# Optimization experiments

Hardware: AMD Instinct MI355X
Metric: run time of the kernel (lower is better)

Reference implementation:

```python
import jax, jax.numpy as jnp
import numpy as np

B, LEN, D, N = 512, 128, 96, 128   # batch, time steps, obs dim, latent dim
NBLOCKS = 5                        # iResNet blocks in encoder/decoder


def expm_fixed(M, squarings=6, order=12):
    """Differentiable matrix exponential: scaling-and-squaring + Taylor-Horner.
    Equivalent to torch.matrix_exp for the well-conditioned skew-symmetric
    A*dt kernels used here (||A*dt|| << 2^squarings)."""
    M = M / (2.0 ** squarings)
    I = jnp.eye(M.shape[-1], dtype=M.dtype)
    P = I
    for k in range(order, 0, -1):  # Horner: I + M(I + M/2(I + ...))
        P = I + (M @ P) / k
    for _ in range(squarings):
        P = P @ P
    return P


def setup_inputs() -> dict:
    key = jax.random.key(0)
    ks = jax.random.split(key, 16)
    # strictly increasing timestamps shared across the batch
    T = jnp.cumsum(0.01 + 0.15 * jax.random.uniform(ks[0], (LEN,), dtype=jnp.float32))
    X = jax.random.normal(ks[1], (B, LEN, D), dtype=jnp.float32)
    mask = jax.random.bernoulli(ks[2], 0.5, (B, LEN, D))  # True = observed
    # skew-symmetric system kernel (kernel_initialization='skew-symmetric')
    W = jax.random.normal(ks[3], (N, N), dtype=jnp.float32) / np.sqrt(N)
    A = 0.5 * (W - W.T)
    # linear embedding d->n and projection n->d
    W_emb = jax.random.normal(ks[4], (N, D), dtype=jnp.float32) / np.sqrt(D)
    b_emb = jnp.zeros((N,), jnp.float32)
    W_proj = jax.random.normal(ks[5], (D, N), dtype=jnp.float32) / np.sqrt(N)
    b_proj = jnp.zeros((D,), jnp.float32)
    # iResNet encoder/decoder: 5 residual blocks of Linear->ReLU->Linear,
    # weights scaled small to mimic the spectral-norm contraction constraint
    cs = 0.5 / np.sqrt(N)
    enc_W1 = jax.random.normal(ks[6], (NBLOCKS, N, N), dtype=jnp.float32) * cs
    enc_b1 = jnp.zeros((NBLOCKS, N), jnp.float32)
    enc_W2 = jax.random.normal(ks[7], (NBLOCKS, N, N), dtype=jnp.float32) * cs
    enc_b2 = jnp.zeros((NBLOCKS, N), jnp.float32)
    dec_W1 = jax.random.normal(ks[8], (NBLOCKS, N, N), dtype=jnp.float32) * cs
    dec_b1 = jnp.zeros((NBLOCKS, N), jnp.float32)
    dec_W2 = jax.random.normal(ks[9], (NBLOCKS, N, N), dtype=jnp.float32) * cs
    dec_b2 = jnp.zeros((NBLOCKS, N), jnp.float32)
    # GRUCell filter: input = concat([xtilde, mask]) (2D features), hidden = D
    s = 1.0 / np.sqrt(D)
    W_ih = jax.random.uniform(ks[10], (3 * D, 2 * D), jnp.float32, -s, s)
    W_hh = jax.random.uniform(ks[11], (3 * D, D), jnp.float32, -s, s)
    b_ih = jax.random.uniform(ks[12], (3 * D,), jnp.float32, -s, s)
    b_hh = jax.random.uniform(ks[13], (3 * D,), jnp.float32, -s, s)
    return {"T": T, "X": X, "mask": mask, "A": A,
            "W_emb": W_emb, "b_emb": b_emb, "W_proj": W_proj, "b_proj": b_proj,
            "enc_W1": enc_W1, "enc_b1": enc_b1, "enc_W2": enc_W2, "enc_b2": enc_b2,
            "dec_W1": dec_W1, "dec_b1": dec_b1, "dec_W2": dec_W2, "dec_b2": dec_b2,
            "W_ih": W_ih, "W_hh": W_hh, "b_ih": b_ih, "b_hh": b_hh}


def reference(T, X, mask, A, W_emb, b_emb, W_proj, b_proj,
              enc_W1, enc_b1, enc_W2, enc_b2,
              dec_W1, dec_b1, dec_W2, dec_b2,
              W_ih, W_hh, b_ih, b_hh):
    def resnet(z, Ws1, bs1, Ws2, bs2):
        for i in range(NBLOCKS):  # fixed small depth
            z = z + jax.nn.relu(z @ Ws1[i].T + bs1[i]) @ Ws2[i].T + bs2[i]
        return z

    def gru(x, h):  # torch.nn.GRUCell math
        gi = x @ W_ih.T + b_ih
        gh = h @ W_hh.T + b_hh
        ir, iz, inn = jnp.split(gi, 3, axis=-1)
        hr, hz, hn = jnp.split(gh, 3, axis=-1)
        r = jax.nn.sigmoid(ir + hr)
        zg = jax.nn.sigmoid(iz + hz)
        ng = jnp.tanh(inn + r * hn)
        return (1.0 - zg) * ng + zg * h

    embed = lambda x: x @ W_emb.T + b_emb
    project = lambda z: z @ W_proj.T + b_proj

    dt = jnp.concatenate([jnp.zeros((1,), T.dtype), jnp.diff(T)])  # (LEN,)
    Xs = jnp.moveaxis(X, 1, 0)      # (LEN, B, D)
    Ms = jnp.moveaxis(mask, 1, 0)   # (LEN, B, D)

    # initial latent state from zero estimate
    z0 = resnet(embed(jnp.zeros((B, D), X.dtype)), enc_W1, enc_b1, enc_W2, enc_b2)

    def step(z, inp):
        dti, xi, mi = inp
        expAdt = expm_fixed(A * dti)                         # (N, N)
        zhat_pre = z @ expAdt.T                              # ODE propagate
        xhat_pre = project(resnet(zhat_pre, dec_W1, dec_b1, dec_W2, dec_b2))
        xtilde = jnp.where(mi, xi, xhat_pre)                 # impute unobserved
        u = jnp.concatenate([xtilde, mi.astype(xi.dtype)], axis=-1)  # concat_mask
        xhat_post = gru(u, xhat_pre)                         # filter update
        z_next = resnet(embed(xhat_post), enc_W1, enc_b1, enc_W2, enc_b2)
        return z_next, xhat_post

    _, Xhat = jax.lax.scan(step, z0, (dt, Xs, Ms))
    return jnp.moveaxis(Xhat, 0, 1)  # (B, LEN, D)
```

## Files before the change

### kernel.cpp

```cpp
#include <hip/hip_runtime.h>
#include <hip/hip_bf16.h>


#define NBATCH 512
#define TLEN 128
#define DDIM 96
#define NDIM 128
#define NBLK 5
#define TAYLOR 8

typedef unsigned short u16;
typedef unsigned int u32;

__device__ __forceinline__ float bf2f(u16 u){ union{u32 i; float f;} v; v.i=((u32)u)<<16; return v.f; }
__device__ __forceinline__ float lo2f(u32 w){ union{u32 i; float f;} v; v.i=w<<16; return v.f; }
__device__ __forceinline__ float hi2f(u32 w){ union{u32 i; float f;} v; v.i=w&0xFFFF0000u; return v.f; }

template<int FM>
__device__ __forceinline__ float ldf(const void* p, int i){
  if constexpr (FM==1) return ((const float*)p)[i];
  else return bf2f(((const u16*)p)[i]);
}

struct __align__(16) SMState {
  float e[NDIM];
  float V0[NDIM];
  float V1[NDIM];
  float zh[NDIM];
  float h[NDIM];
  float xpre[DDIM];
  float u[2*DDIM];
  float gi[3*DDIM];
  float gh[3*DDIM];
  float xpost[DDIM];
};

#define A_STRIDE_E 136

template<int FM, int S, int NO, bool WL, class EPI>
__device__ __forceinline__ void mv(const void* __restrict__ Wg, const u16* __restrict__ Wl,
                                   const int ldw, const float* __restrict__ in,
                                   const int kq, const int j0, EPI epi)
{
  constexpr int NC = S/8;
  float a[S];
  {
    const float* p = in + 8*kq;
#pragma unroll
    for (int ci=0; ci<NC; ci++){
      float4 v0 = *(const float4*)(p + 32*ci);
      float4 v1 = *(const float4*)(p + 32*ci + 4);
      a[8*ci+0]=v0.x; a[8*ci+1]=v0.y; a[8*ci+2]=v0.z; a[8*ci+3]=v0.w;
      a[8*ci+4]=v1.x; a[8*ci+5]=v1.y; a[8*ci+6]=v1.z; a[8*ci+7]=v1.w;
    }
  }
  constexpr int P = (NO+63)/64;
  constexpr bool full = (NO%64==0);
#pragma unroll
  for (int pp=0; pp<P; pp++){
    const int j = pp*64 + j0;
    const bool act = full || (j < NO);
    float ac0=0.f, ac1=0.f, ac2=0.f, ac3=0.f;
    if (act){
      if constexpr (WL){
        const char* wr = (const char*)Wl + 2*(size_t)j*A_STRIDE_E + 16*kq;
#pragma unroll
        for (int ci=0; ci<NC; ci++){
          const uint4 w = *(const uint4*)(wr + 64*ci);
          float f;
          f=lo2f(w.x); ac0=fmaf(f,a[8*ci+0],ac0);
          f=hi2f(w.x); ac1=fmaf(f,a[8*ci+1],ac1);
          f=lo2f(w.y); ac2=fmaf(f,a[8*ci+2],ac2);
          f=hi2f(w.y); ac3=fmaf(f,a[8*ci+3],ac3);
          f=lo2f(w.z); ac0=fmaf(f,a[8*ci+4],ac0);
          f=hi2f(w.z); ac1=fmaf(f,a[8*ci+5],ac1);
          f=lo2f(w.w); ac2=fmaf(f,a[8*ci+6],ac2);
          f=hi2f(w.w); ac3=fmaf(f,a[8*ci+7],ac3);
        }
      } else if constexpr (FM==1){
        const float* wr = (const float*)Wg + (size_t)j*ldw + 8*kq;
#pragma unroll
        for (int ci=0; ci<NC; ci++){
          const float4 w0 = *(const float4*)(wr + 32*ci);
          const float4 w1 = *(const float4*)(wr + 32*ci + 4);
          ac0=fmaf(w0.x,a[8*ci+0],ac0); ac1=fmaf(w0.y,a[8*ci+1],ac1);
          ac2=fmaf(w0.z,a[8*ci+2],ac2); ac3=fmaf(w0.w,a[8*ci+3],ac3);
          ac0=fmaf(w1.x,a[8*ci+4],ac0); ac1=fmaf(w1.y,a[8*ci+5],ac1);
          ac2=fmaf(w1.z,a[8*ci+6],ac2); ac3=fmaf(w1.w,a[8*ci+7],ac3);
        }
      } else {
        const u16* wr = (const u16*)Wg + (size_t)j*ldw + 8*kq;
#pragma unroll
        for (int ci=0; ci<NC; ci++){
          const uint4 w = *(const uint4*)(wr + 32*ci);
          float f;
          f=lo2f(w.x); ac0=fmaf(f,a[8*ci+0],ac0);
          f=hi2f(w.x); ac1=fmaf(f,a[8*ci+1],ac1);
          f=lo2f(w.y); ac2=fmaf(f,a[8*ci+2],ac2);
          f=hi2f(w.y); ac3=fmaf(f,a[8*ci+3],ac3);
          f=lo2f(w.z); ac0=fmaf(f,a[8*ci+4],ac0);
          f=hi2f(w.z); ac1=fmaf(f,a[8*ci+5],ac1);
          f=lo2f(w.w); ac2=fmaf(f,a[8*ci+6],ac2);
          f=hi2f(w.w); ac3=fmaf(f,a[8*ci+7],ac3);
        }
      }
    }
    float acc = (ac0+ac1)+(ac2+ac3);
    acc += __shfl_xor(acc,1,64); acc += __shfl_xor(acc,2,64);
    if (act && kq==0) epi(j, acc);
  }
  __syncthreads();
}

template<int FM>
__device__ __forceinline__ void run_all(
    SMState& sm, u16* Ash, const int mode,
    const void* Tp, const void* Xp, const void* Mp, const void* Ap,
    const void* Wemb, const void* bemb, const void* Wproj, const void* bproj,
    const void* eW1, const void* eb1, const void* eW2, const void* eb2,
    const void* dW1, const void* db1, const void* dW2, const void* db2,
    const void* Wih, const void* Whh, const void* bih, const void* bhh,
    void* Out)
{
  const int tid  = threadIdx.x;
  const int lane = tid & 63;
  const int kq   = lane & 3;
  const int j0   = (tid>>6)*16 + (lane>>2);
  const int r0   = blockIdx.x;
  constexpr int WB = NDIM*NDIM*(FM?4:2);

  if constexpr (FM==0){
    const uint4* src = (const uint4*)Ap;
    for (int i=tid; i<2048; i+=256){
      const int row = i>>4, c = i&15;
      *(uint4*)((char*)Ash + 2*(size_t)row*A_STRIDE_E + 16*c) = src[i];
    }
  }

  if (tid < NDIM) sm.e[tid] = ldf<FM>(bemb, tid);
  __syncthreads();
#pragma unroll 1
  for (int ib=0; ib<NBLK; ib++){
    const void* W1 = (const char*)eW1 + (size_t)ib*WB;
    const void* W2 = (const char*)eW2 + (size_t)ib*WB;
    const int bo = ib*NDIM;
    mv<FM,32,128,false>(W1, nullptr, NDIM, sm.e, kq, j0, [&](int j,float s){
      sm.h[j]=fmaxf(s+ldf<FM>(eb1,bo+j),0.f); });
    mv<FM,32,128,false>(W2, nullptr, NDIM, sm.h, kq, j0, [&](int j,float s){
      sm.e[j]+=s+ldf<FM>(eb2,bo+j); });
  }

#pragma unroll 1
  for (int t=0; t<TLEN; t++){
    float dtv = 0.f;
    if (t > 0) dtv = ldf<FM>(Tp,t) - ldf<FM>(Tp,t-1);

    if (tid < NDIM){ const float z = sm.e[tid]; sm.V0[tid]=z; sm.zh[tid]=z; }
    __syncthreads();

#pragma unroll 1
    for (int k=1; k<=TAYLOR; k++){
      const float sc = dtv / (float)k;
      const float* Vin = (k&1) ? sm.V0 : sm.V1;
      float*      Vout = (k&1) ? sm.V1 : sm.V0;
      if constexpr (FM==0){
        mv<FM,32,128,true>(nullptr, Ash, NDIM, Vin, kq, j0, [&](int j,float s){
          const float v=s*sc; Vout[j]=v; sm.zh[j]+=v; });
      } else {
        mv<FM,32,128,false>(Ap, nullptr, NDIM, Vin, kq, j0, [&](int j,float s){
          const float v=s*sc; Vout[j]=v; sm.zh[j]+=v; });
      }
    }

#pragma unroll 1
    for (int ib=0; ib<NBLK; ib++){
      const void* W1 = (const char*)dW1 + (size_t)ib*WB;
      const void* W2 = (const char*)dW2 + (size_t)ib*WB;
      const int bo = ib*NDIM;
      mv<FM,32,128,false>(W1, nullptr, NDIM, sm.zh, kq, j0, [&](int j,float s){
        sm.h[j]=fmaxf(s+ldf<FM>(db1,bo+j),0.f); });
      mv<FM,32,128,false>(W2, nullptr, NDIM, sm.h, kq, j0, [&](int j,float s){
        sm.zh[j]+=s+ldf<FM>(db2,bo+j); });
    }

    mv<FM,32,96,false>(Wproj, nullptr, NDIM, sm.zh, kq, j0, [&](int j,float s){
      sm.xpre[j]=s+ldf<FM>(bproj,j); });

    if (tid < DDIM){
      const int d = tid;
      const size_t idx = (size_t)r0*TLEN*DDIM + (size_t)t*DDIM + d;
      bool m;
      if      (mode==0) m = ((const u16*)Mp)[idx] != 0;
      else if (mode==1) m = ((const u32*)Mp)[idx] != 0;
      else if (mode==2) m = ((const unsigned char*)Mp)[idx] != 0;
      else              m = ((const int*)Mp)[idx] != 0;
      const float xv = ldf<FM>(Xp, (int)idx);
      sm.u[d]        = m ? xv : sm.xpre[d];
      sm.u[DDIM + d] = m ? 1.f : 0.f;
    }
    __syncthreads();

    mv<FM,48,288,false>(Wih, nullptr, 2*DDIM, sm.u, kq, j0, [&](int j,float s){
      sm.gi[j]=s+ldf<FM>(bih,j); });
    mv<FM,24,288,false>(Whh, nullptr, DDIM, sm.xpre, kq, j0, [&](int j,float s){
      sm.gh[j]=s+ldf<FM>(bhh,j); });

    if (tid < DDIM){
      const int d = tid;
      const float ir=sm.gi[d], iz=sm.gi[DDIM+d], in_=sm.gi[2*DDIM+d];
      const float hr=sm.gh[d], hz=sm.gh[DDIM+d], hn=sm.gh[2*DDIM+d];
      const float rg = 1.f/(1.f+__expf(-(ir+hr)));
      const float zg = 1.f/(1.f+__expf(-(iz+hz)));
      const float ag = in_ + rg*hn;
      const float e2 = __expf(2.f*ag);
      const float ng = 1.f - 2.f/(e2+1.f);
      const float xp = sm.xpre[d];
      const float xq = (1.f-zg)*ng + zg*xp;
      sm.xpost[d] = xq;
      const size_t idx = (size_t)r0*TLEN*DDIM + (size_t)t*DDIM + d;
      if constexpr (FM==1) ((float*)Out)[idx] = xq;
      else ((__hip_bfloat16*)Out)[idx] = __float2bfloat16(xq);
    }
    __syncthreads();

    mv<FM,24,128,false>(Wemb, nullptr, DDIM, sm.xpost, kq, j0, [&](int j,float s){
      sm.e[j]=s+ldf<FM>(bemb,j); });

#pragma unroll 1
    for (int ib=0; ib<NBLK; ib++){
      const void* W1 = (const char*)eW1 + (size_t)ib*WB;
      const void* W2 = (const char*)eW2 + (size_t)ib*WB;
      const int bo = ib*NDIM;
      mv<FM,32,128,false>(W1, nullptr, NDIM, sm.e, kq, j0, [&](int j,float s){
        sm.h[j]=fmaxf(s+ldf<FM>(eb1,bo+j),0.f); });
      mv<FM,32,128,false>(W2, nullptr, NDIM, sm.h, kq, j0, [&](int j,float s){
        sm.e[j]+=s+ldf<FM>(eb2,bo+j); });
    }
  }
}

__global__ __launch_bounds__(256, 2)
void linode_kernel(const void* Tp, const void* Xp, const void* Mp, const void* Ap,
                   const void* Wemb, const void* bemb, const void* Wproj, const void* bproj,
                   const void* eW1, const void* eb1, const void* eW2, const void* eb2,
                   const void* dW1, const void* db1, const void* dW2, const void* db2,
                   const void* Wih, const void* Whh, const void* bih, const void* bhh,
                   void* Out)
{
  __shared__ SMState sm;
  __shared__ __align__(16) u16 Ash[NDIM*A_STRIDE_E];
  __shared__ int s_f[4];
  const int tid = threadIdx.x;

  if (tid < 4) s_f[tid] = 0;
  __syncthreads();
  if (tid == 0){
    int all0 = 1;
    for (int k=0; k<8; k++) all0 &= (((const u32*)Ap)[129*k] == 0u);
    s_f[3] = all0;
  }
  {
    const u32* mw = (const u32*)Mp;
    int fb=0, ff=0, fg=0;
    for (int i=tid; i<2048; i+=256){
      const u32 w = mw[i];
      if (w == 0x3F803F80u) fb = 1;
      if ((w&0xFFFFu)==0x3F80u || (w>>16)==0x3F80u) ff = 1;
      if (w > 1u) fg = 1;
    }
    if (fb) atomicOr(&s_f[0],1);
    if (ff) atomicOr(&s_f[1],1);
    if (fg) atomicOr(&s_f[2],1);
  }
  __syncthreads();
  const int mode = s_f[0] ? 0 : (s_f[1] ? 1 : (s_f[2] ? 2 : 3));
  const int f32m = s_f[3];
  __syncthreads();

  if (f32m)
    run_all<1>(sm, Ash, mode, Tp, Xp, Mp, Ap, Wemb, bemb, Wproj, bproj,
               eW1, eb1, eW2, eb2, dW1, db1, dW2, db2, Wih, Whh, bih, bhh, Out);
  else
    run_all<0>(sm, Ash, mode, Tp, Xp, Mp, Ap, Wemb, bemb, Wproj, bproj,
               eW1, eb1, eW2, eb2, dW1, db1, dW2, db2, Wih, Whh, bih, bhh, Out);
}

extern "C" void kernel_launch(void* const* d_in, const int* in_sizes, int n_in,
                              void* d_out, int out_size, void* d_ws, size_t ws_size,
                              hipStream_t stream)
{
  (void)in_sizes; (void)n_in; (void)out_size; (void)d_ws; (void)ws_size;
  hipLaunchKernelGGL(linode_kernel, dim3(NBATCH), dim3(256), 0, stream,
                     d_in[0], d_in[1], d_in[2], d_in[3],
                     d_in[4], d_in[5], d_in[6], d_in[7],
                     d_in[8], d_in[9], d_in[10], d_in[11],
                     d_in[12], d_in[13], d_in[14], d_in[15],
                     d_in[16], d_in[17], d_in[18], d_in[19],
                     d_out);
}
```

Baseline: 5.743 ms.

## Precompute per-step matrix exponentials in a separate kernel and widen blocks to 512 threads

Adds a kernel that builds each time step's truncated-Taylor expm(A*dt) in bf16 into workspace. The main recurrence then replaces eight Taylor matvecs per step with a single matvec against the precomputed matrix. The main kernel moves from 256 to 512 threads per block, which halves the output rows per thread in mv. All biases are staged into shared memory, and mask and X loads are issued early in each step. The cost is an extra launch plus a 4 MB workspace read per step, and the propagator is rounded to bf16, which changes numerics slightly.

```diff
diff --git a/kernel.cpp b/kernel.cpp
--- a/kernel.cpp
+++ b/kernel.cpp
@@ -8,6 +8,7 @@
 #define NDIM 128
 #define NBLK 5
 #define TAYLOR 8
+#define A_STRIDE_E 136
 
 typedef unsigned short u16;
 typedef unsigned int u32;
@@ -15,12 +16,23 @@
 __device__ __forceinline__ float bf2f(u16 u){ union{u32 i; float f;} v; v.i=((u32)u)<<16; return v.f; }
 __device__ __forceinline__ float lo2f(u32 w){ union{u32 i; float f;} v; v.i=w<<16; return v.f; }
 __device__ __forceinline__ float hi2f(u32 w){ union{u32 i; float f;} v; v.i=w&0xFFFF0000u; return v.f; }
+__device__ __forceinline__ u16 f2bf(float x){ union{float f;u32 i;} v; v.f=x; u32 r=v.i+0x7FFF+((v.i>>16)&1); return (u16)(r>>16); }
 
 template<int FM>
 __device__ __forceinline__ float ldf(const void* p, int i){
   if constexpr (FM==1) return ((const float*)p)[i];
   else return bf2f(((const u16*)p)[i]);
 }
+
+#define OEB1 0
+#define OEB2 640
+#define ODB1 1280
+#define ODB2 1920
+#define OBEMB 2560
+#define OBPROJ 2688
+#define OBIH 2784
+#define OBHH 3072
+#define NBIAS 3360
 
 struct __align__(16) SMState {
   float e[NDIM];
@@ -35,7 +47,93 @@
   float xpost[DDIM];
 };
 
-#define A_STRIDE_E 136
+__global__ __launch_bounds__(256, 1)
+void expm_kernel(const void* Tp, const void* Ap, u16* Ews)
+{
+  __shared__ int sf;
+  __shared__ __align__(16) u16 Ash2[NDIM*A_STRIDE_E];
+  __shared__ __align__(16) float V[2][64*132];
+  const int tid = threadIdx.x;
+  if (tid==0){
+    int all0=1;
+    for (int k=0;k<8;k++) all0 &= (((const u32*)Ap)[129*k]==0u);
+    sf = all0;
+  }
+  __syncthreads();
+  if (sf) return;
+
+  const int t = blockIdx.x >> 1, half = blockIdx.x & 1;
+  float dtv = 0.f;
+  if (t>0) dtv = bf2f(((const u16*)Tp)[t]) - bf2f(((const u16*)Tp)[t-1]);
+  {
+    const uint4* src = (const uint4*)Ap;
+    for (int i=tid;i<2048;i+=256){
+      const int row=i>>4, c=i&15;
+      *(uint4*)((char*)Ash2 + 2*(size_t)row*A_STRIDE_E + 16*c) = src[i];
+    }
+  }
+  const int c2 = tid & 31, rh = tid >> 5;
+  const int j0r = rh*16;
+  const int lc0 = 2*c2, lc1 = lc0+1;
+  const int gc0 = half*64 + lc0, gc1 = gc0+1;
+
+  float acc0[16], acc1[16];
+#pragma unroll
+  for (int jj=0;jj<16;jj++){
+    const int kk = j0r+jj;
+    const float i0 = (kk==gc0)?1.f:0.f, i1 = (kk==gc1)?1.f:0.f;
+    acc0[jj]=i0; acc1[jj]=i1;
+    V[0][lc0*132+kk]=i0; V[0][lc1*132+kk]=i1;
+  }
+  __syncthreads();
+  int cur=0;
+#pragma unroll 1
+  for (int k=1;k<=8;k++){
+    const float sc = dtv/(float)k;
+    float o0[16], o1[16];
+#pragma unroll
+    for (int jj=0;jj<16;jj++){ o0[jj]=0.f; o1[jj]=0.f; }
+#pragma unroll 1
+    for (int kb=0;kb<16;kb++){
+      const float4 va0 = *(const float4*)&V[cur][lc0*132+kb*8];
+      const float4 vb0 = *(const float4*)&V[cur][lc0*132+kb*8+4];
+      const float4 va1 = *(const float4*)&V[cur][lc1*132+kb*8];
+      const float4 vb1 = *(const float4*)&V[cur][lc1*132+kb*8+4];
+      const float v0[8]={va0.x,va0.y,va0.z,va0.w,vb0.x,vb0.y,vb0.z,vb0.w};
+      const float v1[8]={va1.x,va1.y,va1.z,va1.w,vb1.x,vb1.y,vb1.z,vb1.w};
+#pragma unroll
+      for (int jj=0;jj<16;jj++){
+        const int j = j0r+jj;
+        const uint4 w = *(const uint4*)((const char*)Ash2 + 2*(size_t)j*A_STRIDE_E + 16*kb);
+        float f;
+        f=lo2f(w.x); o0[jj]=fmaf(f,v0[0],o0[jj]); o1[jj]=fmaf(f,v1[0],o1[jj]);
+        f=hi2f(w.x); o0[jj]=fmaf(f,v0[1],o0[jj]); o1[jj]=fmaf(f,v1[1],o1[jj]);
+        f=lo2f(w.y); o0[jj]=fmaf(f,v0[2],o0[jj]); o1[jj]=fmaf(f,v1[2],o1[jj]);
+        f=hi2f(w.y); o0[jj]=fmaf(f,v0[3],o0[jj]); o1[jj]=fmaf(f,v1[3],o1[jj]);
+        f=lo2f(w.z); o0[jj]=fmaf(f,v0[4],o0[jj]); o1[jj]=fmaf(f,v1[4],o1[jj]);
+        f=hi2f(w.z); o0[jj]=fmaf(f,v0[5],o0[jj]); o1[jj]=fmaf(f,v1[5],o1[jj]);
+        f=lo2f(w.w); o0[jj]=fmaf(f,v0[6],o0[jj]); o1[jj]=fmaf(f,v1[6],o1[jj]);
+        f=hi2f(w.w); o0[jj]=fmaf(f,v0[7],o0[jj]); o1[jj]=fmaf(f,v1[7],o1[jj]);
+      }
+    }
+    __syncthreads();
+#pragma unroll
+    for (int jj=0;jj<16;jj++){
+      const int j=j0r+jj;
+      const float s0=o0[jj]*sc, s1=o1[jj]*sc;
+      acc0[jj]+=s0; acc1[jj]+=s1;
+      V[cur^1][lc0*132+j]=s0; V[cur^1][lc1*132+j]=s1;
+    }
+    __syncthreads();
+    cur^=1;
+  }
+#pragma unroll
+  for (int jj=0;jj<16;jj++){
+    const int j=j0r+jj;
+    const u32 pk = (u32)f2bf(acc0[jj]) | ((u32)f2bf(acc1[jj])<<16);
+    *((u32*)(Ews + (size_t)t*NDIM*NDIM + (size_t)j*NDIM + gc0)) = pk;
+  }
+}
 
 template<int FM, int S, int NO, bool WL, class EPI>
 __device__ __forceinline__ void mv(const void* __restrict__ Wg, const u16* __restrict__ Wl,
@@ -43,6 +141,8 @@
                                    const int kq, const int j0, EPI epi)
 {
   constexpr int NC = S/8;
+  constexpr int P = (NO+127)/128;
+  constexpr bool full = (NO%128==0);
   float a[S];
   {
     const float* p = in + 8*kq;
@@ -54,11 +154,9 @@
       a[8*ci+4]=v1.x; a[8*ci+5]=v1.y; a[8*ci+6]=v1.z; a[8*ci+7]=v1.w;
     }
   }
-  constexpr int P = (NO+63)/64;
-  constexpr bool full = (NO%64==0);
 #pragma unroll
   for (int pp=0; pp<P; pp++){
-    const int j = pp*64 + j0;
+    const int j = pp*128 + j0;
     const bool act = full || (j < NO);
     float ac0=0.f, ac1=0.f, ac2=0.f, ac3=0.f;
     if (act){
@@ -113,14 +211,19 @@
 }
 
 template<int FM>
+__device__ __forceinline__ void stage_b(const void* src, float* dst, int n, int tid){
+  for (int i=tid;i<n;i+=512) dst[i] = ldf<FM>(src,i);
+}
+
+template<int FM>
 __device__ __forceinline__ void run_all(
-    SMState& sm, u16* Ash, const int mode,
+    SMState& sm, float* smb, u16* Ash, const int mode, const int useE,
     const void* Tp, const void* Xp, const void* Mp, const void* Ap,
     const void* Wemb, const void* bemb, const void* Wproj, const void* bproj,
     const void* eW1, const void* eb1, const void* eW2, const void* eb2,
     const void* dW1, const void* db1, const void* dW2, const void* db2,
     const void* Wih, const void* Whh, const void* bih, const void* bhh,
-    void* Out)
+    const u16* Ep, void* Out)
 {
   const int tid  = threadIdx.x;
   const int lane = tid & 63;
@@ -129,15 +232,24 @@
   const int r0   = blockIdx.x;
   constexpr int WB = NDIM*NDIM*(FM?4:2);
 
-  if constexpr (FM==0){
+  stage_b<FM>(eb1, smb+OEB1, NBLK*NDIM, tid);
+  stage_b<FM>(eb2, smb+OEB2, NBLK*NDIM, tid);
+  stage_b<FM>(db1, smb+ODB1, NBLK*NDIM, tid);
+  stage_b<FM>(db2, smb+ODB2, NBLK*NDIM, tid);
+  stage_b<FM>(bemb, smb+OBEMB, NDIM, tid);
+  stage_b<FM>(bproj, smb+OBPROJ, DDIM, tid);
+  stage_b<FM>(bih, smb+OBIH, 3*DDIM, tid);
+  stage_b<FM>(bhh, smb+OBHH, 3*DDIM, tid);
+  if (FM==0 && !useE){
     const uint4* src = (const uint4*)Ap;
-    for (int i=tid; i<2048; i+=256){
-      const int row = i>>4, c = i&15;
+    for (int i=tid;i<2048;i+=512){
+      const int row=i>>4, c=i&15;
       *(uint4*)((char*)Ash + 2*(size_t)row*A_STRIDE_E + 16*c) = src[i];
     }
   }
-
-  if (tid < NDIM) sm.e[tid] = ldf<FM>(bemb, tid);
+  __syncthreads();
+
+  if (tid < NDIM) sm.e[tid] = smb[OBEMB+tid];
   __syncthreads();
 #pragma unroll 1
   for (int ib=0; ib<NBLK; ib++){
@@ -145,30 +257,44 @@
     const void* W2 = (const char*)eW2 + (size_t)ib*WB;
     const int bo = ib*NDIM;
     mv<FM,32,128,false>(W1, nullptr, NDIM, sm.e, kq, j0, [&](int j,float s){
-      sm.h[j]=fmaxf(s+ldf<FM>(eb1,bo+j),0.f); });
+      sm.h[j]=fmaxf(s+smb[OEB1+bo+j],0.f); });
     mv<FM,32,128,false>(W2, nullptr, NDIM, sm.h, kq, j0, [&](int j,float s){
-      sm.e[j]+=s+ldf<FM>(eb2,bo+j); });
+      sm.e[j]+=s+smb[OEB2+bo+j]; });
   }
 
 #pragma unroll 1
   for (int t=0; t<TLEN; t++){
-    float dtv = 0.f;
-    if (t > 0) dtv = ldf<FM>(Tp,t) - ldf<FM>(Tp,t-1);
-
-    if (tid < NDIM){ const float z = sm.e[tid]; sm.V0[tid]=z; sm.zh[tid]=z; }
-    __syncthreads();
-
-#pragma unroll 1
-    for (int k=1; k<=TAYLOR; k++){
-      const float sc = dtv / (float)k;
-      const float* Vin = (k&1) ? sm.V0 : sm.V1;
-      float*      Vout = (k&1) ? sm.V1 : sm.V0;
-      if constexpr (FM==0){
-        mv<FM,32,128,true>(nullptr, Ash, NDIM, Vin, kq, j0, [&](int j,float s){
-          const float v=s*sc; Vout[j]=v; sm.zh[j]+=v; });
-      } else {
-        mv<FM,32,128,false>(Ap, nullptr, NDIM, Vin, kq, j0, [&](int j,float s){
-          const float v=s*sc; Vout[j]=v; sm.zh[j]+=v; });
+    float xv_r = 0.f; int m_r = 0;
+    if (tid < DDIM){
+      const size_t idx = (size_t)r0*TLEN*DDIM + (size_t)t*DDIM + tid;
+      if      (mode==0) m_r = ((const u16*)Mp)[idx] != 0;
+      else if (mode==1) m_r = ((const u32*)Mp)[idx] != 0;
+      else if (mode==2) m_r = ((const unsigned char*)Mp)[idx] != 0;
+      else              m_r = ((const int*)Mp)[idx] != 0;
+      xv_r = ldf<FM>(Xp, (int)idx);
+    }
+
+    if (FM==0 && useE){
+      const u16* Et = Ep + (size_t)t*NDIM*NDIM;
+      mv<0,32,128,false>(Et, nullptr, NDIM, sm.e, kq, j0, [&](int j,float s){
+        sm.zh[j]=s; });
+    } else {
+      float dtv = 0.f;
+      if (t>0) dtv = ldf<FM>(Tp,t) - ldf<FM>(Tp,t-1);
+      if (tid < NDIM){ const float z=sm.e[tid]; sm.V0[tid]=z; sm.zh[tid]=z; }
+      __syncthreads();
+#pragma unroll 1
+      for (int k=1;k<=TAYLOR;k++){
+        const float sc = dtv/(float)k;
+        const float* Vin = (k&1)?sm.V0:sm.V1;
+        float*      Vout = (k&1)?sm.V1:sm.V0;
+        if constexpr (FM==0){
+          mv<0,32,128,true>(nullptr, Ash, NDIM, Vin, kq, j0, [&](int j,float s){
+            const float v=s*sc; Vout[j]=v; sm.zh[j]+=v; });
+        } else {
+          mv<1,32,128,false>(Ap, nullptr, NDIM, Vin, kq, j0, [&](int j,float s){
+            const float v=s*sc; Vout[j]=v; sm.zh[j]+=v; });
+        }
       }
     }
 
@@ -178,32 +304,24 @@
       const void* W2 = (const char*)dW2 + (size_t)ib*WB;
       const int bo = ib*NDIM;
       mv<FM,32,128,false>(W1, nullptr, NDIM, sm.zh, kq, j0, [&](int j,float s){
-        sm.h[j]=fmaxf(s+ldf<FM>(db1,bo+j),0.f); });
+        sm.h[j]=fmaxf(s+smb[ODB1+bo+j],0.f); });
       mv<FM,32,128,false>(W2, nullptr, NDIM, sm.h, kq, j0, [&](int j,float s){
-        sm.zh[j]+=s+ldf<FM>(db2,bo+j); });
+        sm.zh[j]+=s+smb[ODB2+bo+j]; });
     }
 
     mv<FM,32,96,false>(Wproj, nullptr, NDIM, sm.zh, kq, j0, [&](int j,float s){
-      sm.xpre[j]=s+ldf<FM>(bproj,j); });
+      sm.xpre[j]=s+smb[OBPROJ+j]; });
 
     if (tid < DDIM){
-      const int d = tid;
-      const size_t idx = (size_t)r0*TLEN*DDIM + (size_t)t*DDIM + d;
-      bool m;
-      if      (mode==0) m = ((const u16*)Mp)[idx] != 0;
-      else if (mode==1) m = ((const u32*)Mp)[idx] != 0;
-      else if (mode==2) m = ((const unsigned char*)Mp)[idx] != 0;
-      else              m = ((const int*)Mp)[idx] != 0;
-      const float xv = ldf<FM>(Xp, (int)idx);
-      sm.u[d]        = m ? xv : sm.xpre[d];
-      sm.u[DDIM + d] = m ? 1.f : 0.f;
+      sm.u[tid]      = m_r ? xv_r : sm.xpre[tid];
+      sm.u[DDIM+tid] = m_r ? 1.f : 0.f;
     }
     __syncthreads();
 
     mv<FM,48,288,false>(Wih, nullptr, 2*DDIM, sm.u, kq, j0, [&](int j,float s){
-      sm.gi[j]=s+ldf<FM>(bih,j); });
+      sm.gi[j]=s+smb[OBIH+j]; });
     mv<FM,24,288,false>(Whh, nullptr, DDIM, sm.xpre, kq, j0, [&](int j,float s){
-      sm.gh[j]=s+ldf<FM>(bhh,j); });
+      sm.gh[j]=s+smb[OBHH+j]; });
 
     if (tid < DDIM){
       const int d = tid;
@@ -224,7 +342,7 @@
     __syncthreads();
 
     mv<FM,24,128,false>(Wemb, nullptr, DDIM, sm.xpost, kq, j0, [&](int j,float s){
-      sm.e[j]=s+ldf<FM>(bemb,j); });
+      sm.e[j]=s+smb[OBEMB+j]; });
 
 #pragma unroll 1
     for (int ib=0; ib<NBLK; ib++){
@@ -232,22 +350,23 @@
       const void* W2 = (const char*)eW2 + (size_t)ib*WB;
       const int bo = ib*NDIM;
       mv<FM,32,128,false>(W1, nullptr, NDIM, sm.e, kq, j0, [&](int j,float s){
-        sm.h[j]=fmaxf(s+ldf<FM>(eb1,bo+j),0.f); });
+        sm.h[j]=fmaxf(s+smb[OEB1+bo+j],0.f); });
       mv<FM,32,128,false>(W2, nullptr, NDIM, sm.h, kq, j0, [&](int j,float s){
-        sm.e[j]+=s+ldf<FM>(eb2,bo+j); });
-    }
-  }
-}
-
-__global__ __launch_bounds__(256, 2)
+        sm.e[j]+=s+smb[OEB2+bo+j]; });
+    }
+  }
+}
+
+__global__ __launch_bounds__(512, 4)
 void linode_kernel(const void* Tp, const void* Xp, const void* Mp, const void* Ap,
                    const void* Wemb, const void* bemb, const void* Wproj, const void* bproj,
                    const void* eW1, const void* eb1, const void* eW2, const void* eb2,
                    const void* dW1, const void* db1, const void* dW2, const void* db2,
                    const void* Wih, const void* Whh, const void* bih, const void* bhh,
-                   void* Out)
+                   const u16* Ep, const int useE, void* Out)
 {
   __shared__ SMState sm;
+  __shared__ float smb[NBIAS];
   __shared__ __align__(16) u16 Ash[NDIM*A_STRIDE_E];
   __shared__ int s_f[4];
   const int tid = threadIdx.x;
@@ -256,13 +375,13 @@
   __syncthreads();
   if (tid == 0){
     int all0 = 1;
-    for (int k=0; k<8; k++) all0 &= (((const u32*)Ap)[129*k] == 0u);
+    for (int k=0;k<8;k++) all0 &= (((const u32*)Ap)[129*k] == 0u);
     s_f[3] = all0;
   }
   {
     const u32* mw = (const u32*)Mp;
     int fb=0, ff=0, fg=0;
-    for (int i=tid; i<2048; i+=256){
+    for (int i=tid;i<2048;i+=512){
       const u32 w = mw[i];
       if (w == 0x3F803F80u) fb = 1;
       if ((w&0xFFFFu)==0x3F80u || (w>>16)==0x3F80u) ff = 1;
@@ -278,23 +397,27 @@
   __syncthreads();
 
   if (f32m)
-    run_all<1>(sm, Ash, mode, Tp, Xp, Mp, Ap, Wemb, bemb, Wproj, bproj,
-               eW1, eb1, eW2, eb2, dW1, db1, dW2, db2, Wih, Whh, bih, bhh, Out);
+    run_all<1>(sm, smb, Ash, mode, useE, Tp, Xp, Mp, Ap, Wemb, bemb, Wproj, bproj,
+               eW1, eb1, eW2, eb2, dW1, db1, dW2, db2, Wih, Whh, bih, bhh, Ep, Out);
   else
-    run_all<0>(sm, Ash, mode, Tp, Xp, Mp, Ap, Wemb, bemb, Wproj, bproj,
-               eW1, eb1, eW2, eb2, dW1, db1, dW2, db2, Wih, Whh, bih, bhh, Out);
+    run_all<0>(sm, smb, Ash, mode, useE, Tp, Xp, Mp, Ap, Wemb, bemb, Wproj, bproj,
+               eW1, eb1, eW2, eb2, dW1, db1, dW2, db2, Wih, Whh, bih, bhh, Ep, Out);
 }
 
 extern "C" void kernel_launch(void* const* d_in, const int* in_sizes, int n_in,
                               void* d_out, int out_size, void* d_ws, size_t ws_size,
                               hipStream_t stream)
 {
-  (void)in_sizes; (void)n_in; (void)out_size; (void)d_ws; (void)ws_size;
-  hipLaunchKernelGGL(linode_kernel, dim3(NBATCH), dim3(256), 0, stream,
+  (void)in_sizes; (void)n_in; (void)out_size;
+  const int useE = (ws_size >= (size_t)TLEN*NDIM*NDIM*2) ? 1 : 0;
+  if (useE)
+    hipLaunchKernelGGL(expm_kernel, dim3(2*TLEN), dim3(256), 0, stream,
+                       d_in[0], d_in[3], (u16*)d_ws);
+  hipLaunchKernelGGL(linode_kernel, dim3(NBATCH), dim3(512), 0, stream,
                      d_in[0], d_in[1], d_in[2], d_in[3],
                      d_in[4], d_in[5], d_in[6], d_in[7],
                      d_in[8], d_in[9], d_in[10], d_in[11],
                      d_in[12], d_in[13], d_in[14], d_in[15],
                      d_in[16], d_in[17], d_in[18], d_in[19],
-                     d_out);
-}
+                     (const u16*)d_ws, useE, d_out);
+}
```

New measurement: 5.207 ms. 9.3% less time.
